# Kernel tuning notes

Measured on AMD Instinct MI355X. Metric: run time of the kernel, lower is better.

## Reference

```python
import jax, jax.numpy as jnp
import numpy as np

EMBED = 1024
HEADS = 16
HEAD_DIM = EMBED // HEADS
LN_EPS = 1e-5


def _layer_norm(x, g, b):
    m = jnp.mean(x, axis=-1, keepdims=True)
    v = jnp.mean((x - m) ** 2, axis=-1, keepdims=True)
    return (x - m) / jnp.sqrt(v + LN_EPS) * g + b


def _rope(x):
    # x: (b, H, n, D); standard rotary: freqs repeated (cat(freqs, freqs)), rotate_half
    D = x.shape[-1]
    n = x.shape[2]
    inv_freq = 1.0 / (10000.0 ** (jnp.arange(0, D, 2, dtype=jnp.float32) / D))
    freqs = jnp.arange(n, dtype=jnp.float32)[:, None] * inv_freq[None, :]  # (n, D/2)
    emb = jnp.concatenate([freqs, freqs], axis=-1)  # (n, D)
    cos, sin = jnp.cos(emb), jnp.sin(emb)
    rot = jnp.concatenate([-x[..., D // 2:], x[..., : D // 2]], axis=-1)
    return x * cos + rot * sin


def setup_inputs() -> dict:
    key = jax.random.key(0)
    ks = jax.random.split(key, 8)
    E = EMBED
    s_in = 1.0 / np.sqrt(E)
    return {
        "x": jax.random.normal(ks[0], (2, 2048, E), dtype=jnp.float32),
        "in_proj_w": jax.random.uniform(ks[1], (3 * E, E), jnp.float32, -s_in, s_in),
        "in_proj_b": jnp.zeros((3 * E,), jnp.float32),
        "out_proj_w": jax.random.uniform(ks[2], (E, E), jnp.float32, -s_in, s_in),
        "out_proj_b": jnp.zeros((E,), jnp.float32),
        "geglu_w": jax.random.uniform(ks[3], (2 * E, E), jnp.float32, -s_in, s_in),
        "geglu_b": jnp.zeros((2 * E,), jnp.float32),
        "ln1_g": jnp.ones((E,), jnp.float32),
        "ln1_b": jnp.zeros((E,), jnp.float32),
        "ln2_g": jnp.ones((E,), jnp.float32),
        "ln2_b": jnp.zeros((E,), jnp.float32),
    }


def reference(x, in_proj_w, in_proj_b, out_proj_w, out_proj_b,
              geglu_w, geglu_b, ln1_g, ln1_b, ln2_g, ln2_b):
    b, n, E = x.shape
    H, D = HEADS, HEAD_DIM

    # RoPE applied to raw x (q = k = v = x in the module)
    xh = x.reshape(b, n, H, D).transpose(0, 2, 1, 3)  # (b,H,n,D)
    qr = _rope(xh)
    kr = qr  # q and k are identical pre-projection
    q = qr.transpose(0, 2, 1, 3).reshape(b, n, E)
    k = kr.transpose(0, 2, 1, 3).reshape(b, n, E)
    v = x

    # MultiheadAttention (batch-first semantics): in-proj, per-head SDPA, out-proj
    w_q, w_k, w_v = jnp.split(in_proj_w, 3, axis=0)
    b_q, b_k, b_v = jnp.split(in_proj_b, 3, axis=0)
    qp = (q @ w_q.T + b_q).reshape(b, n, H, D).transpose(0, 2, 1, 3)
    kp = (k @ w_k.T + b_k).reshape(b, n, H, D).transpose(0, 2, 1, 3)
    vp = (v @ w_v.T + b_v).reshape(b, n, H, D).transpose(0, 2, 1, 3)
    scores = jnp.einsum("bhqd,bhkd->bhqk", qp, kp) / jnp.sqrt(jnp.float32(D))
    attn = jax.nn.softmax(scores, axis=-1)
    ctx = jnp.einsum("bhqk,bhkd->bhqd", attn, vp)
    ctx = ctx.transpose(0, 2, 1, 3).reshape(b, n, E)
    attn_out = ctx @ out_proj_w.T + out_proj_b

    # residual + LN1
    h = _layer_norm(x + attn_out, ln1_g, ln1_b)

    # GeGLU: Linear(E -> 2E), chunk, value * gelu(gate) (exact erf gelu like torch)
    proj = h @ geglu_w.T + geglu_b
    val, gate = jnp.split(proj, 2, axis=-1)
    fc_out = val * jax.nn.gelu(gate, approximate=False)

    # residual + LN2
    return _layer_norm(h + fc_out, ln2_g, ln2_b)
```

## Files before the change

kernel.cpp:

```cpp
#include <hip/hip_runtime.h>


typedef __bf16 bf16;
typedef bf16 bf16x8 __attribute__((ext_vector_type(8)));
typedef bf16 bf16x4 __attribute__((ext_vector_type(4)));
typedef float f32x4 __attribute__((ext_vector_type(4)));
typedef float f32x16 __attribute__((ext_vector_type(16)));

#define EMB 1024
#define SEQ 2048
#define NTOK 4096
#define NH 16
#define HD 64

__device__ __forceinline__ f32x4 mfma16(bf16x8 a, bf16x8 b, f32x4 c) {
  return __builtin_amdgcn_mfma_f32_16x16x32_bf16(a, b, c, 0, 0, 0);
}
__device__ __forceinline__ f32x16 mfma32(bf16x8 a, bf16x8 b, f32x16 c) {
  return __builtin_amdgcn_mfma_f32_32x32x16_bf16(a, b, c, 0, 0, 0);
}

__device__ __forceinline__ void gll16(const void* g, void* l) {
  __builtin_amdgcn_global_load_lds(
      (const __attribute__((address_space(1))) void*)g,
      (__attribute__((address_space(3))) void*)l, 16, 0, 0);
}


__global__ __launch_bounds__(256) void rope_cast(
    const float* __restrict__ x, bf16* __restrict__ xb, bf16* __restrict__ qr) {
  int idx = blockIdx.x * 256 + threadIdx.x;
  int row = idx >> 9;
  int i = idx & 511;
  int h = i >> 5, d2 = i & 31;
  int pos = row & (SEQ - 1);
  int c0 = h * HD + d2;
  size_t base = (size_t)row * EMB;
  float x0 = x[base + c0], x1 = x[base + c0 + 32];
  float invf = exp2f(-(float)d2 * 0.4152410118609203f);
  float ang = (float)pos * invf;
  float sn, cs;
  sincosf(ang, &sn, &cs);
  qr[base + c0] = (bf16)(x0 * cs - x1 * sn);
  qr[base + c0 + 32] = (bf16)(x1 * cs + x0 * sn);
  xb[base + c0] = (bf16)x0;
  xb[base + c0 + 32] = (bf16)x1;
}

__global__ __launch_bounds__(256) void cast_w(
    const float* __restrict__ w, bf16* __restrict__ o, int n) {
  int i = (blockIdx.x * 256 + threadIdx.x) * 4;
  if (i < n) {
    float4 f = *(const float4*)(w + i);
    o[i] = (bf16)f.x; o[i + 1] = (bf16)f.y;
    o[i + 2] = (bf16)f.z; o[i + 3] = (bf16)f.w;
  }
}

__global__ __launch_bounds__(256) void gemm_in(
    const bf16* __restrict__ Aq, const bf16* __restrict__ Ax,
    const bf16* __restrict__ W, const float* __restrict__ bias,
    bf16* __restrict__ qk, bf16* __restrict__ vT) {
  __shared__ bf16 As[128 * 32];
  __shared__ bf16 Bs[128 * 32];
  const int tid = threadIdx.x, lane = tid & 63, wave = tid >> 6;
  const int quad = lane >> 4, l16 = lane & 15;
  const int m0 = blockIdx.y * 128, n0 = blockIdx.x * 128;
  const bf16* A = (n0 < 2048) ? Aq : Ax;
  const int K = 1024;
  const int wm = (wave >> 1) * 64, wn = (wave & 1) * 64;
  const int srow = wave * 32 + (lane >> 2);
  const int scol = (lane & 3) * 8;
  f32x4 acc[4][4] = {};
  for (int k0 = 0; k0 < K; k0 += 32) {
    __syncthreads();
    gll16(A + (size_t)(m0 + srow) * K + k0 + scol, As + wave * 1024);
    gll16(A + (size_t)(m0 + srow + 16) * K + k0 + scol, As + wave * 1024 + 512);
    gll16(W + (size_t)(n0 + srow) * K + k0 + scol, Bs + wave * 1024);
    gll16(W + (size_t)(n0 + srow + 16) * K + k0 + scol, Bs + wave * 1024 + 512);
    __syncthreads();
    bf16x8 af[4], bw[4];
#pragma unroll
    for (int t = 0; t < 4; ++t) {
      af[t] = *(const bf16x8*)(As + (wm + t * 16 + l16) * 32 + quad * 8);
      bw[t] = *(const bf16x8*)(Bs + (wn + t * 16 + l16) * 32 + quad * 8);
    }
#pragma unroll
    for (int mt = 0; mt < 4; ++mt)
#pragma unroll
      for (int nt = 0; nt < 4; ++nt)
        acc[mt][nt] = mfma16(af[mt], bw[nt], acc[mt][nt]);
  }
  if (n0 < 2048) {
#pragma unroll
    for (int mt = 0; mt < 4; ++mt)
      for (int nt = 0; nt < 4; ++nt) {
        const int n = n0 + wn + nt * 16 + l16;
        const float bv = bias[n];
#pragma unroll
        for (int r = 0; r < 4; ++r) {
          const int m = m0 + wm + mt * 16 + quad * 4 + r;
          qk[(size_t)m * 2048 + n] = (bf16)(acc[mt][nt][r] + bv);
        }
      }
  } else {
#pragma unroll
    for (int mt = 0; mt < 4; ++mt)
      for (int nt = 0; nt < 4; ++nt) {
        const int n = n0 + wn + nt * 16 + l16;
        const float bv = bias[n];
        const int m = m0 + wm + mt * 16 + quad * 4;
        const int bb = m >> 11, s = m & 2047;
        bf16x4 pk;
#pragma unroll
        for (int r = 0; r < 4; ++r) pk[r] = (bf16)(acc[mt][nt][r] + bv);
        *(bf16x4*)(vT + (((size_t)bb * 1024 + (n - 2048)) << 11) + s) = pk;
      }
  }
}

__global__ __launch_bounds__(256) void gemm_bt(
    const bf16* __restrict__ A, const bf16* __restrict__ W,
    const float* __restrict__ bias,
    float* __restrict__ outF, bf16* __restrict__ outB,
    int M, int N, int K) {
  __shared__ bf16 As[128 * 32];
  __shared__ bf16 Bs[128 * 32];
  const int tid = threadIdx.x, lane = tid & 63, wave = tid >> 6;
  const int quad = lane >> 4, l16 = lane & 15;
  const int m0 = blockIdx.y * 128, n0 = blockIdx.x * 128;
  const int wm = (wave >> 1) * 64, wn = (wave & 1) * 64;
  const int srow = wave * 32 + (lane >> 2);
  const int scol = (lane & 3) * 8;
  f32x4 acc[4][4] = {};
  for (int k0 = 0; k0 < K; k0 += 32) {
    __syncthreads();
    gll16(A + (size_t)(m0 + srow) * K + k0 + scol, As + wave * 1024);
    gll16(A + (size_t)(m0 + srow + 16) * K + k0 + scol, As + wave * 1024 + 512);
    gll16(W + (size_t)(n0 + srow) * K + k0 + scol, Bs + wave * 1024);
    gll16(W + (size_t)(n0 + srow + 16) * K + k0 + scol, Bs + wave * 1024 + 512);
    __syncthreads();
    bf16x8 af[4], bw[4];
#pragma unroll
    for (int t = 0; t < 4; ++t) {
      af[t] = *(const bf16x8*)(As + (wm + t * 16 + l16) * 32 + quad * 8);
      bw[t] = *(const bf16x8*)(Bs + (wn + t * 16 + l16) * 32 + quad * 8);
    }
#pragma unroll
    for (int mt = 0; mt < 4; ++mt)
#pragma unroll
      for (int nt = 0; nt < 4; ++nt)
        acc[mt][nt] = mfma16(af[mt], bw[nt], acc[mt][nt]);
  }
#pragma unroll
  for (int mt = 0; mt < 4; ++mt)
    for (int nt = 0; nt < 4; ++nt) {
      const int n = n0 + wn + nt * 16 + l16;
      const float bv = bias ? bias[n] : 0.0f;
#pragma unroll
      for (int r = 0; r < 4; ++r) {
        const int m = m0 + wm + mt * 16 + quad * 4 + r;
        const float v = acc[mt][nt][r] + bv;
        if (outF) outF[(size_t)m * N + n] = v;
        if (outB) outB[(size_t)m * N + n] = (bf16)v;
      }
    }
}

__global__ __launch_bounds__(256) void gemm_bt64(
    const bf16* __restrict__ A, const bf16* __restrict__ W,
    const float* __restrict__ bias, float* __restrict__ outF,
    int M, int N, int K) {
  __shared__ bf16 As[128 * 32];
  __shared__ bf16 Bs[64 * 32];
  const int tid = threadIdx.x, lane = tid & 63, wave = tid >> 6;
  const int quad = lane >> 4, l16 = lane & 15;
  const int m0 = blockIdx.y * 128, n0 = blockIdx.x * 64;
  const int wm = (wave >> 1) * 64, wn = (wave & 1) * 32;
  const int srow = wave * 32 + (lane >> 2);
  const int srowB = wave * 16 + (lane >> 2);
  const int scol = (lane & 3) * 8;
  f32x4 acc[4][2] = {};
  for (int k0 = 0; k0 < K; k0 += 32) {
    __syncthreads();
    gll16(A + (size_t)(m0 + srow) * K + k0 + scol, As + wave * 1024);
    gll16(A + (size_t)(m0 + srow + 16) * K + k0 + scol, As + wave * 1024 + 512);
    gll16(W + (size_t)(n0 + srowB) * K + k0 + scol, Bs + wave * 512);
    __syncthreads();
    bf16x8 af[4], bw[2];
#pragma unroll
    for (int t = 0; t < 4; ++t)
      af[t] = *(const bf16x8*)(As + (wm + t * 16 + l16) * 32 + quad * 8);
#pragma unroll
    for (int t = 0; t < 2; ++t)
      bw[t] = *(const bf16x8*)(Bs + (wn + t * 16 + l16) * 32 + quad * 8);
#pragma unroll
    for (int mt = 0; mt < 4; ++mt)
#pragma unroll
      for (int nt = 0; nt < 2; ++nt)
        acc[mt][nt] = mfma16(af[mt], bw[nt], acc[mt][nt]);
  }
#pragma unroll
  for (int mt = 0; mt < 4; ++mt)
    for (int nt = 0; nt < 2; ++nt) {
      const int n = n0 + wn + nt * 16 + l16;
      const float bv = bias[n];
#pragma unroll
      for (int r = 0; r < 4; ++r) {
        const int m = m0 + wm + mt * 16 + quad * 4 + r;
        outF[(size_t)m * N + n] = acc[mt][nt][r] + bv;
      }
    }
}

__global__ __launch_bounds__(256) void attn4(
    const bf16* __restrict__ QK, const bf16* __restrict__ VT,
    bf16* __restrict__ ctx) {
  __shared__ __align__(16) bf16 Ks[64 * 64];
  __shared__ __align__(16) bf16 Vs[64 * 64];
  __shared__ __align__(16) bf16 Ps[4 * 32 * 64];
  __shared__ float Linv[4][32];
  const int tid = threadIdx.x, lane = tid & 63, wave = tid >> 6;
  const int hi = lane >> 5, l31 = lane & 31, l7 = lane & 7;
  const int qt = blockIdx.x, h = blockIdx.y, b = blockIdx.z;

  bf16x8 qf[4];
  {
    const int qrow = qt * 128 + wave * 32 + l31;
    const bf16* qp = QK + (size_t)(b * SEQ + qrow) * 2048 + h * HD + hi * 8;
#pragma unroll
    for (int t = 0; t < 4; ++t) {
      bf16x8 v = *(const bf16x8*)(qp + t * 16);
#pragma unroll
      for (int j = 0; j < 8; ++j) v[j] = (bf16)((float)v[j] * 0.125f);
      qf[t] = v;
    }
  }
  f32x16 o0 = {}, o1 = {};
  float lpart = 0.0f;

  const bf16* kg = QK + (size_t)(b * SEQ) * 2048 + 1024 + h * HD;
  const bf16* vg = VT + ((size_t)(b * NH + h) * HD) * 2048;
  bf16* pw = Ps + wave * 2048;

  for (int kb = 0; kb < SEQ; kb += 64) {
    __syncthreads();
#pragma unroll
    for (int p = 0; p < 2; ++p) {
      const int c = p * 256 + tid;
      const int row = c >> 3, c16 = c & 7;
      const int sw = row * 64 + ((c16 ^ (row & 7)) * 8);
      *(bf16x8*)(Ks + sw) = *(const bf16x8*)(kg + (size_t)(kb + row) * 2048 + c16 * 8);
      *(bf16x8*)(Vs + sw) = *(const bf16x8*)(vg + (size_t)row * 2048 + kb + c16 * 8);
    }
    __syncthreads();
    f32x16 s0 = {}, s1 = {};
#pragma unroll
    for (int t = 0; t < 4; ++t) {
      const int swc = ((t * 2 + hi) ^ l7) * 8;
      bf16x8 k0 = *(const bf16x8*)(Ks + l31 * 64 + swc);
      bf16x8 k1 = *(const bf16x8*)(Ks + (32 + l31) * 64 + swc);
      s0 = mfma32(k0, qf[t], s0);
      s1 = mfma32(k1, qf[t], s1);
    }
#pragma unroll
    for (int kc = 0; kc < 2; ++kc) {
      const f32x16& sv = kc ? s1 : s0;
#pragma unroll
      for (int g = 0; g < 4; ++g) {
        bf16x4 pk;
#pragma unroll
        for (int j = 0; j < 4; ++j) {
          float e = __expf(sv[g * 4 + j]);
          lpart += e;
          pk[j] = (bf16)e;
        }
        *(bf16x4*)(pw + l31 * 64 + (((kc * 4 + g) ^ l7) * 8) + hi * 4) = pk;
      }
    }
#pragma unroll
    for (int t2 = 0; t2 < 4; ++t2) {
      const int swc = ((t2 * 2 + hi) ^ l7) * 8;
      bf16x8 pf = *(const bf16x8*)(pw + l31 * 64 + swc);
      bf16x8 v0 = *(const bf16x8*)(Vs + l31 * 64 + swc);
      bf16x8 v1 = *(const bf16x8*)(Vs + (32 + l31) * 64 + swc);
      o0 = mfma32(pf, v0, o0);
      o1 = mfma32(pf, v1, o1);
    }
  }
  float ltot = lpart + __shfl_xor(lpart, 32, 64);
  if (lane < 32) Linv[wave][lane] = 1.0f / ltot;
#pragma unroll
  for (int r = 0; r < 16; ++r) {
    const int qloc = (r & 3) + 8 * (r >> 2) + 4 * hi;
    const float inv = Linv[wave][qloc];
    const int qrow = qt * 128 + wave * 32 + qloc;
    bf16* cp = ctx + (size_t)(b * SEQ + qrow) * EMB + h * HD;
    cp[l31] = (bf16)(o0[r] * inv);
    cp[32 + l31] = (bf16)(o1[r] * inv);
  }
}

__global__ __launch_bounds__(256) void ln1_k(
    const float* __restrict__ x, const float* __restrict__ ao,
    const float* __restrict__ g, const float* __restrict__ bta,
    float* __restrict__ hF, bf16* __restrict__ hB) {
  int row = blockIdx.x, tid = threadIdx.x;
  const float* xr = x + (size_t)row * EMB;
  const float* ar = ao + (size_t)row * EMB;
  float v[4], s = 0.0f, s2 = 0.0f;
#pragma unroll
  for (int i = 0; i < 4; ++i) {
    float t = xr[tid + i * 256] + ar[tid + i * 256];
    v[i] = t; s += t; s2 += t * t;
  }
#pragma unroll
  for (int off = 1; off < 64; off <<= 1) {
    s += __shfl_xor(s, off, 64);
    s2 += __shfl_xor(s2, off, 64);
  }
  __shared__ float red[8];
  int wave = tid >> 6, lane = tid & 63;
  if (lane == 0) { red[wave] = s; red[4 + wave] = s2; }
  __syncthreads();
  s = red[0] + red[1] + red[2] + red[3];
  s2 = red[4] + red[5] + red[6] + red[7];
  float mean = s * (1.0f / EMB);
  float var = s2 * (1.0f / EMB) - mean * mean;
  float inv = rsqrtf(var + 1e-5f);
#pragma unroll
  for (int i = 0; i < 4; ++i) {
    int c = tid + i * 256;
    float t = (v[i] - mean) * inv * g[c] + bta[c];
    hF[(size_t)row * EMB + c] = t;
    hB[(size_t)row * EMB + c] = (bf16)t;
  }
}

__global__ __launch_bounds__(256) void geglu_ln2(
    const float* __restrict__ h, const bf16* __restrict__ proj,
    const float* __restrict__ g, const float* __restrict__ bta,
    float* __restrict__ out) {
  int row = blockIdx.x, tid = threadIdx.x;
  const float* hr = h + (size_t)row * EMB;
  const bf16* pr = proj + (size_t)row * 2048;
  float v[4], s = 0.0f, s2 = 0.0f;
#pragma unroll
  for (int i = 0; i < 4; ++i) {
    int c = tid + i * 256;
    float val = (float)pr[c];
    float gate = (float)pr[1024 + c];
    float ge = 0.5f * gate * (1.0f + erff(gate * 0.70710678f));
    float t = hr[c] + val * ge;
    v[i] = t; s += t; s2 += t * t;
  }
#pragma unroll
  for (int off = 1; off < 64; off <<= 1) {
    s += __shfl_xor(s, off, 64);
    s2 += __shfl_xor(s2, off, 64);
  }
  __shared__ float red[8];
  int wave = tid >> 6, lane = tid & 63;
  if (lane == 0) { red[wave] = s; red[4 + wave] = s2; }
  __syncthreads();
  s = red[0] + red[1] + red[2] + red[3];
  s2 = red[4] + red[5] + red[6] + red[7];
  float mean = s * (1.0f / EMB);
  float var = s2 * (1.0f / EMB) - mean * mean;
  float inv = rsqrtf(var + 1e-5f);
#pragma unroll
  for (int i = 0; i < 4; ++i) {
    int c = tid + i * 256;
    out[(size_t)row * EMB + c] = (v[i] - mean) * inv * g[c] + bta[c];
  }
}

extern "C" void kernel_launch(void* const* d_in, const int* in_sizes, int n_in,
                              void* d_out, int out_size, void* d_ws, size_t ws_size,
                              hipStream_t stream) {
  const float* x = (const float*)d_in[0];
  const float* inW = (const float*)d_in[1];
  const float* inB = (const float*)d_in[2];
  const float* outW = (const float*)d_in[3];
  const float* opB = (const float*)d_in[4];
  const float* ggW = (const float*)d_in[5];
  const float* ggB = (const float*)d_in[6];
  const float* g1 = (const float*)d_in[7];
  const float* b1 = (const float*)d_in[8];
  const float* g2 = (const float*)d_in[9];
  const float* b2 = (const float*)d_in[10];
  float* out = (float*)d_out;
  char* ws = (char*)d_ws;
  const size_t MB = 1ull << 20;
  bf16* xb = (bf16*)(ws);
  bf16* qr = (bf16*)(ws + 8 * MB);
  bf16* ctx = (bf16*)(ws + 8 * MB);
  bf16* wI = (bf16*)(ws + 16 * MB);
  bf16* wO = (bf16*)(ws + 22 * MB);
  bf16* wG = (bf16*)(ws + 24 * MB);
  bf16* qk = (bf16*)(ws + 28 * MB);
  bf16* projB = (bf16*)(ws + 28 * MB);
  bf16* vbT = (bf16*)(ws + 44 * MB);
  float* ao = (float*)(ws + 44 * MB);
  bf16* hB = (bf16*)(ws + 60 * MB);

  rope_cast<<<NTOK * 512 / 256, 256, 0, stream>>>(x, xb, qr);
  cast_w<<<(3072 * 1024 / 4) / 256, 256, 0, stream>>>(inW, wI, 3072 * 1024);
  cast_w<<<(1024 * 1024 / 4) / 256, 256, 0, stream>>>(outW, wO, 1024 * 1024);
  cast_w<<<(2048 * 1024 / 4) / 256, 256, 0, stream>>>(ggW, wG, 2048 * 1024);
  gemm_in<<<dim3(24, 32), 256, 0, stream>>>(qr, xb, wI, inB, qk, vbT);
  attn4<<<dim3(16, 16, 2), 256, 0, stream>>>(qk, vbT, ctx);
  gemm_bt64<<<dim3(16, 32), 256, 0, stream>>>(ctx, wO, opB, ao,
                                              NTOK, 1024, 1024);
  ln1_k<<<NTOK, 256, 0, stream>>>(x, ao, g1, b1, ao, hB);
  gemm_bt<<<dim3(16, 32), 256, 0, stream>>>(hB, wG, ggB, nullptr, projB,
                                            NTOK, 2048, 1024);
  geglu_ln2<<<NTOK, 256, 0, stream>>>(ao, projB, g2, b2, out);
}
```

Before: 294.7 us.

## Prefetch K/V tiles into registers and pass P via lane shuffles

The attention kernel now loads the next K/V tile from global memory into registers while the current tile is processed, overlapping global latency with MFMA work. It also drops the per-wave P scratch buffer in LDS and rebuilds the P operand for the PV matmul from the score accumulators using cross-half-wave shuffles. This removes LDS round-trips and shrinks LDS use, at the cost of extra registers and shuffle instructions.

Result: faster. 277.4 us (-5.9%).

```diff
diff --git a/kernel.cpp b/kernel.cpp
--- a/kernel.cpp
+++ b/kernel.cpp
@@ -24,6 +24,12 @@
   __builtin_amdgcn_global_load_lds(
       (const __attribute__((address_space(1))) void*)g,
       (__attribute__((address_space(3))) void*)l, 16, 0, 0);
+}
+
+__device__ __forceinline__ unsigned pk2(float a, float b) {
+  union { bf16 h[2]; unsigned u; } t;
+  t.h[0] = (bf16)a; t.h[1] = (bf16)b;
+  return t.u;
 }
 
 
@@ -111,10 +117,10 @@
         const float bv = bias[n];
         const int m = m0 + wm + mt * 16 + quad * 4;
         const int bb = m >> 11, s = m & 2047;
-        bf16x4 pk;
-#pragma unroll
-        for (int r = 0; r < 4; ++r) pk[r] = (bf16)(acc[mt][nt][r] + bv);
-        *(bf16x4*)(vT + (((size_t)bb * 1024 + (n - 2048)) << 11) + s) = pk;
+        bf16x4 pkv;
+#pragma unroll
+        for (int r = 0; r < 4; ++r) pkv[r] = (bf16)(acc[mt][nt][r] + bv);
+        *(bf16x4*)(vT + (((size_t)bb * 1024 + (n - 2048)) << 11) + s) = pkv;
       }
   }
 }
@@ -213,12 +219,11 @@
     }
 }
 
-__global__ __launch_bounds__(256) void attn4(
+__global__ __launch_bounds__(256) void attn6(
     const bf16* __restrict__ QK, const bf16* __restrict__ VT,
     bf16* __restrict__ ctx) {
   __shared__ __align__(16) bf16 Ks[64 * 64];
   __shared__ __align__(16) bf16 Vs[64 * 64];
-  __shared__ __align__(16) bf16 Ps[4 * 32 * 64];
   __shared__ float Linv[4][32];
   const int tid = threadIdx.x, lane = tid & 63, wave = tid >> 6;
   const int hi = lane >> 5, l31 = lane & 31, l7 = lane & 7;
@@ -239,21 +244,37 @@
   f32x16 o0 = {}, o1 = {};
   float lpart = 0.0f;
 
-  const bf16* kg = QK + (size_t)(b * SEQ) * 2048 + 1024 + h * HD;
-  const bf16* vg = VT + ((size_t)(b * NH + h) * HD) * 2048;
-  bf16* pw = Ps + wave * 2048;
+  const int srow = tid >> 3;
+  const int sc16 = tid & 7;
+  const bf16* kg = QK + (size_t)(b * SEQ) * 2048 + 1024 + h * HD + sc16 * 8;
+  const bf16* vg = VT + ((size_t)(b * NH + h) * HD) * 2048 + sc16 * 8;
+
+  bf16x8 kcur[2], vcur[2];
+#pragma unroll
+  for (int p = 0; p < 2; ++p) {
+    const int row = p * 32 + srow;
+    kcur[p] = *(const bf16x8*)(kg + (size_t)row * 2048);
+    vcur[p] = *(const bf16x8*)(vg + (size_t)row * 2048);
+  }
 
   for (int kb = 0; kb < SEQ; kb += 64) {
     __syncthreads();
 #pragma unroll
     for (int p = 0; p < 2; ++p) {
-      const int c = p * 256 + tid;
-      const int row = c >> 3, c16 = c & 7;
-      const int sw = row * 64 + ((c16 ^ (row & 7)) * 8);
-      *(bf16x8*)(Ks + sw) = *(const bf16x8*)(kg + (size_t)(kb + row) * 2048 + c16 * 8);
-      *(bf16x8*)(Vs + sw) = *(const bf16x8*)(vg + (size_t)row * 2048 + kb + c16 * 8);
-    }
-    __syncthreads();
+      const int row = p * 32 + srow;
+      const int sw = row * 64 + ((sc16 ^ (row & 7)) * 8);
+      *(bf16x8*)(Ks + sw) = kcur[p];
+      *(bf16x8*)(Vs + sw) = vcur[p];
+    }
+    __syncthreads();
+    if (kb + 64 < SEQ) {
+#pragma unroll
+      for (int p = 0; p < 2; ++p) {
+        const int row = p * 32 + srow;
+        kcur[p] = *(const bf16x8*)(kg + (size_t)(kb + 64 + row) * 2048);
+        vcur[p] = *(const bf16x8*)(vg + (size_t)row * 2048 + kb + 64);
+      }
+    }
     f32x16 s0 = {}, s1 = {};
 #pragma unroll
     for (int t = 0; t < 4; ++t) {
@@ -263,29 +284,39 @@
       s0 = mfma32(k0, qf[t], s0);
       s1 = mfma32(k1, qf[t], s1);
     }
-#pragma unroll
-    for (int kc = 0; kc < 2; ++kc) {
-      const f32x16& sv = kc ? s1 : s0;
-#pragma unroll
-      for (int g = 0; g < 4; ++g) {
-        bf16x4 pk;
-#pragma unroll
-        for (int j = 0; j < 4; ++j) {
-          float e = __expf(sv[g * 4 + j]);
-          lpart += e;
-          pk[j] = (bf16)e;
-        }
-        *(bf16x4*)(pw + l31 * 64 + (((kc * 4 + g) ^ l7) * 8) + hi * 4) = pk;
-      }
-    }
-#pragma unroll
-    for (int t2 = 0; t2 < 4; ++t2) {
-      const int swc = ((t2 * 2 + hi) ^ l7) * 8;
-      bf16x8 pf = *(const bf16x8*)(pw + l31 * 64 + swc);
+    unsigned u[16];
+#pragma unroll
+    for (int g = 0; g < 8; ++g) {
+      const int base = (g & 3) * 4;
+      float e0, e1, e2, e3;
+      if (g < 4) {
+        e0 = __expf(s0[base]); e1 = __expf(s0[base + 1]);
+        e2 = __expf(s0[base + 2]); e3 = __expf(s0[base + 3]);
+      } else {
+        e0 = __expf(s1[base]); e1 = __expf(s1[base + 1]);
+        e2 = __expf(s1[base + 2]); e3 = __expf(s1[base + 3]);
+      }
+      lpart += (e0 + e1) + (e2 + e3);
+      u[g * 2] = pk2(e0, e1);
+      u[g * 2 + 1] = pk2(e2, e3);
+    }
+#pragma unroll
+    for (int kk = 0; kk < 4; ++kk) {
+      const int ub = (kk >> 1) * 8 + (kk & 1) * 4;
+      unsigned sx = hi ? u[ub] : u[ub + 2];
+      unsigned sy = hi ? u[ub + 1] : u[ub + 3];
+      unsigned rx = (unsigned)__shfl_xor((int)sx, 32, 64);
+      unsigned ry = (unsigned)__shfl_xor((int)sy, 32, 64);
+      union { unsigned w[4]; bf16x8 v; } fw;
+      fw.w[0] = hi ? rx : u[ub];
+      fw.w[1] = hi ? ry : u[ub + 1];
+      fw.w[2] = hi ? u[ub + 2] : rx;
+      fw.w[3] = hi ? u[ub + 3] : ry;
+      const int swc = ((kk * 2 + hi) ^ l7) * 8;
       bf16x8 v0 = *(const bf16x8*)(Vs + l31 * 64 + swc);
       bf16x8 v1 = *(const bf16x8*)(Vs + (32 + l31) * 64 + swc);
-      o0 = mfma32(pf, v0, o0);
-      o1 = mfma32(pf, v1, o1);
+      o0 = mfma32(fw.v, v0, o0);
+      o1 = mfma32(fw.v, v1, o1);
     }
   }
   float ltot = lpart + __shfl_xor(lpart, 32, 64);
@@ -409,7 +440,7 @@
   cast_w<<<(1024 * 1024 / 4) / 256, 256, 0, stream>>>(outW, wO, 1024 * 1024);
   cast_w<<<(2048 * 1024 / 4) / 256, 256, 0, stream>>>(ggW, wG, 2048 * 1024);
   gemm_in<<<dim3(24, 32), 256, 0, stream>>>(qr, xb, wI, inB, qk, vbT);
-  attn4<<<dim3(16, 16, 2), 256, 0, stream>>>(qk, vbT, ctx);
+  attn6<<<dim3(16, 16, 2), 256, 0, stream>>>(qk, vbT, ctx);
   gemm_bt64<<<dim3(16, 32), 256, 0, stream>>>(ctx, wO, opB, ao,
                                               NTOK, 1024, 1024);
   ln1_k<<<NTOK, 256, 0, stream>>>(x, ao, g1, b1, ao, hB);
```
